# Optimization experiments

Hardware: AMD Instinct MI355X
Metric: run time of the kernel (lower is better)

The kernel has to match this reference:

```python
import jax, jax.numpy as jnp
import numpy as np

N_NODES = 100000
N_EDGES = 3200000
D_IN = 128
D_OUT = 128


def setup_inputs() -> dict:
    key = jax.random.key(0)
    k1, k2, k3, k4, k5 = jax.random.split(key, 5)
    input_feature = jax.random.normal(k1, (N_NODES, D_IN), dtype=jnp.float32)
    edge_src = jax.random.randint(k2, (N_EDGES,), 0, N_NODES, dtype=jnp.int32)
    edge_dst = jax.random.randint(k3, (N_EDGES,), 0, N_NODES, dtype=jnp.int32)
    edge_vals = jax.random.uniform(k4, (N_EDGES,), dtype=jnp.float32)
    # kaiming-uniform-like init for weight, zeros for bias (as in reset_parameters)
    bound = float(np.sqrt(6.0 / D_IN))
    weight = jax.random.uniform(k5, (D_IN, D_OUT), dtype=jnp.float32,
                                minval=-bound, maxval=bound)
    bias = jnp.zeros((D_OUT,), dtype=jnp.float32)
    return {
        "input_feature": input_feature,
        "edge_src": edge_src,
        "edge_dst": edge_dst,
        "edge_vals": edge_vals,
        "weight": weight,
        "bias": bias,
    }


def reference(input_feature, edge_src, edge_dst, edge_vals, weight, bias):
    # support = X @ W  -> [N, D_OUT]
    support = jnp.matmul(input_feature, weight)
    # sparse.mm(A, support): out[dst] += A[dst, src] * support[src]
    gathered = support[edge_src] * edge_vals[:, None]  # [E, D_OUT]
    output = jax.ops.segment_sum(gathered, edge_dst, num_segments=N_NODES)
    output = output + bias  # bias-add (use_bias=True)
    return output
```

## Files before the change

### kernel.cpp

```cpp
#include <hip/hip_runtime.h>

#define N_NODES 100000
#define N_EDGES 3200000
#define D 128

#define K1C    391
#define CHUNK  4096
#define NCHUNK 782
#define GEMMB  782
#define CAPB   8960

static const size_t OFF_SB    = 0;
static const size_t OFF_REC   = 25600000;
static const size_t OFF_SORT2 = 53626880;
static const size_t OFF_OFFS  = 67640320;
static const size_t OFF_GCUR  = 68040320;

typedef __attribute__((ext_vector_type(8))) short bf16x8;
typedef __attribute__((ext_vector_type(4))) float f32x4;

__device__ __forceinline__ unsigned short f2bf(float f) {
    unsigned u = __float_as_uint(f);
    return (unsigned short)((u + 0x7FFFu + ((u >> 16) & 1u)) >> 16);
}

__global__ __launch_bounds__(512) void part_and_gemm(
        const int* __restrict__ esrc,
        const int* __restrict__ edst,
        const float* __restrict__ eval,
        int* __restrict__ gcursor,
        int2* __restrict__ rec_out,
        const float* __restrict__ X,
        const float* __restrict__ W,
        unsigned* __restrict__ Sb) {
    __shared__ __align__(16) union {
        unsigned short wfrag[8][4][64][8];
        unsigned       stage[8][16][68];
        struct {
            int2 staged[CHUNK];
            unsigned short bkt[CHUNK];
            int hist[K1C];
            int lofs[K1C];
            int gbase[K1C];
            int cur[K1C];
            int wsum[8];
        } p;
    } u;

    const int t    = threadIdx.x;
    const int lane = t & 63;
    const int wave = t >> 6;

    if (blockIdx.x < NCHUNK) {
        const int e0  = blockIdx.x * CHUNK;
        const int cnt = min(CHUNK, N_EDGES - e0);
        const int nq  = cnt >> 2;

        for (int i = t; i < K1C; i += 512) u.p.hist[i] = 0;
        __syncthreads();

        for (int i = t; i < nq; i += 512) {
            int4 d4 = ((const int4*)(edst + e0))[i];
            atomicAdd(&u.p.hist[d4.x >> 8], 1);
            atomicAdd(&u.p.hist[d4.y >> 8], 1);
            atomicAdd(&u.p.hist[d4.z >> 8], 1);
            atomicAdd(&u.p.hist[d4.w >> 8], 1);
        }
        __syncthreads();

        int hv   = (t < K1C) ? u.p.hist[t] : 0;
        int incl = hv;
        for (int off = 1; off < 64; off <<= 1) {
            int uu = __shfl_up(incl, off);
            if (lane >= off) incl += uu;
        }
        if (lane == 63) u.p.wsum[wave] = incl;
        __syncthreads();
        {
            int pre = 0;
            for (int w = 0; w < wave; ++w) pre += u.p.wsum[w];
            if (t < K1C) {
                int excl = pre + incl - hv;
                u.p.lofs[t]  = excl;
                u.p.cur[t]   = excl;
                u.p.gbase[t] = hv ? (t * CAPB + atomicAdd(&gcursor[t], hv)) : 0;
            }
        }
        __syncthreads();

        for (int i = t; i < nq; i += 512) {
            int4   d4 = ((const int4*)(edst + e0))[i];
            int4   s4 = ((const int4*)(esrc + e0))[i];
            float4 v4 = ((const float4*)(eval + e0))[i];
            {
                int b = d4.x >> 8;
                int pos = atomicAdd(&u.p.cur[b], 1);
                u.p.staged[pos] = make_int2(s4.x | ((d4.x & 255) << 17),
                                            __float_as_int(v4.x));
                u.p.bkt[pos] = (unsigned short)b;
            }
            {
                int b = d4.y >> 8;
                int pos = atomicAdd(&u.p.cur[b], 1);
                u.p.staged[pos] = make_int2(s4.y | ((d4.y & 255) << 17),
                                            __float_as_int(v4.y));
                u.p.bkt[pos] = (unsigned short)b;
            }
            {
                int b = d4.z >> 8;
                int pos = atomicAdd(&u.p.cur[b], 1);
                u.p.staged[pos] = make_int2(s4.z | ((d4.z & 255) << 17),
                                            __float_as_int(v4.z));
                u.p.bkt[pos] = (unsigned short)b;
            }
            {
                int b = d4.w >> 8;
                int pos = atomicAdd(&u.p.cur[b], 1);
                u.p.staged[pos] = make_int2(s4.w | ((d4.w & 255) << 17),
                                            __float_as_int(v4.w));
                u.p.bkt[pos] = (unsigned short)b;
            }
        }
        __syncthreads();

        for (int i = t; i < cnt; i += 512) {
            int bb = u.p.bkt[i];
            rec_out[u.p.gbase[bb] + (i - u.p.lofs[bb])] = u.p.staged[i];
        }
    } else {
        const int quad = lane >> 4;
        const int li   = lane & 15;
        const int rowBase = (blockIdx.x - NCHUNK) * 128;

        for (int i = t; i < D * D; i += 512) {
            int k = i >> 7, n = i & 127;
            u.wfrag[n >> 4][k >> 5][((k >> 3) & 3) * 16 + (n & 15)][k & 7] = f2bf(W[i]);
        }
        __syncthreads();

        f32x4 acc[8];
#pragma unroll
        for (int ct = 0; ct < 8; ++ct)
            acc[ct] = (f32x4){0.f, 0.f, 0.f, 0.f};

#pragma unroll
        for (int kt = 0; kt < 4; ++kt) {
            int row = rowBase + wave * 16 + li;
            if (row >= N_NODES) row = N_NODES - 1;
            const float* xp = X + (size_t)row * D + kt * 32 + quad * 8;
            float4 f0 = ((const float4*)xp)[0];
            float4 f1 = ((const float4*)xp)[1];
            bf16x8 a;
            a[0] = (short)f2bf(f0.x); a[1] = (short)f2bf(f0.y);
            a[2] = (short)f2bf(f0.z); a[3] = (short)f2bf(f0.w);
            a[4] = (short)f2bf(f1.x); a[5] = (short)f2bf(f1.y);
            a[6] = (short)f2bf(f1.z); a[7] = (short)f2bf(f1.w);
#pragma unroll
            for (int ct = 0; ct < 8; ++ct) {
                bf16x8 b = *(const bf16x8*)&u.wfrag[ct][kt][lane][0];
                acc[ct] = __builtin_amdgcn_mfma_f32_16x16x32_bf16(a, b, acc[ct], 0, 0, 0);
            }
        }
        __syncthreads();

        unsigned short* sw = (unsigned short*)&u.stage[wave][0][0];
#pragma unroll
        for (int r = 0; r < 4; ++r) {
            int lrow = quad * 4 + r;
#pragma unroll
            for (int ct = 0; ct < 8; ++ct)
                sw[lrow * 136 + ct * 16 + li] = f2bf(acc[ct][r]);
        }
        for (int lrow = 0; lrow < 16; ++lrow) {
            int node = rowBase + wave * 16 + lrow;
            if (node < N_NODES)
                Sb[(size_t)node * 64 + lane] = ((unsigned*)sw)[lrow * 68 + lane];
        }
    }
}

__global__ __launch_bounds__(512) void fine_sort(
        const int2* __restrict__ rec,
        const int* __restrict__ gcnt,
        int* __restrict__ offs,
        unsigned* __restrict__ sorted1) {
    __shared__ int fh[256];
    __shared__ int fcur[256];
    __shared__ int fwsum[4];

    const int c    = blockIdx.x;
    const int t    = threadIdx.x;
    const int lane = t & 63;
    const int beg  = c * CAPB;
    const int bcnt = gcnt[c];
    const int np   = bcnt >> 1;

    if (t < 256) fh[t] = 0;
    __syncthreads();

    for (int i = t; i < np; i += 512) {
        int4 q = ((const int4*)(rec + beg))[i];
        atomicAdd(&fh[(q.x >> 17) & 255], 1);
        atomicAdd(&fh[(q.z >> 17) & 255], 1);
    }
    if (t == 0 && (bcnt & 1))
        atomicAdd(&fh[(rec[beg + bcnt - 1].x >> 17) & 255], 1);
    __syncthreads();

    if (t < 256) {
        int hv   = fh[t];
        int incl = hv;
        for (int off = 1; off < 64; off <<= 1) {
            int uu = __shfl_up(incl, off);
            if (lane >= off) incl += uu;
        }
        if (lane == 63) fwsum[t >> 6] = incl;
        fh[t] = incl - hv;
    }
    __syncthreads();
    if (t < 256) {
        int pre = 0;
        for (int w = 0; w < (t >> 6); ++w) pre += fwsum[w];
        int excl = pre + fh[t];
        int node = c * 256 + t;
        if (node < N_NODES) offs[node] = beg + excl;
        fcur[t] = beg + excl;
    }
    __syncthreads();

    for (int i = t; i < np; i += 512) {
        int4 q = ((const int4*)(rec + beg))[i];
        {
            int dl = (q.x >> 17) & 255;
            int p = atomicAdd(&fcur[dl], 1);
            unsigned vb = f2bf(__int_as_float(q.y));
            sorted1[p] = (unsigned)(q.x & 0x1FFFF) | ((vb & 0x7FFFu) << 17);
        }
        {
            int dl = (q.z >> 17) & 255;
            int p = atomicAdd(&fcur[dl], 1);
            unsigned vb = f2bf(__int_as_float(q.w));
            sorted1[p] = (unsigned)(q.z & 0x1FFFF) | ((vb & 0x7FFFu) << 17);
        }
    }
    if (t == 0 && (bcnt & 1)) {
        int2 q = rec[beg + bcnt - 1];
        int dl = (q.x >> 17) & 255;
        int p = atomicAdd(&fcur[dl], 1);
        unsigned vb = f2bf(__int_as_float(q.y));
        sorted1[p] = (unsigned)(q.x & 0x1FFFF) | ((vb & 0x7FFFu) << 17);
    }
}

#define FMA8(v, p) {                                                         \
    a0 += (v) * __uint_as_float((p).x << 16);                                \
    a1 += (v) * __uint_as_float((p).x & 0xFFFF0000u);                        \
    a2 += (v) * __uint_as_float((p).y << 16);                                \
    a3 += (v) * __uint_as_float((p).y & 0xFFFF0000u);                        \
    a4 += (v) * __uint_as_float((p).z << 16);                                \
    a5 += (v) * __uint_as_float((p).z & 0xFFFF0000u);                        \
    a6 += (v) * __uint_as_float((p).w << 16);                                \
    a7 += (v) * __uint_as_float((p).w & 0xFFFF0000u);                        \
}

__global__ __launch_bounds__(256) void reduce_segments(
        const unsigned* __restrict__ Sb,
        const unsigned* __restrict__ sorted,
        const int* __restrict__ offs,
        const int* __restrict__ gcnt,
        const float* __restrict__ bias,
        float* __restrict__ out) {
    const int lane = threadIdx.x & 63;
    const int node = (blockIdx.x * 256 + threadIdx.x) >> 6;
    if (node >= N_NODES) return;

    const int qr = lane >> 4;
    const int ql = lane & 15;

    const int beg = offs[node];
    const bool blast = ((node & 255) == 255) || (node == N_NODES - 1);
    const int end = blast ? ((node >> 8) * CAPB + gcnt[node >> 8])
                          : offs[node + 1];

    float a0 = 0.f, a1 = 0.f, a2 = 0.f, a3 = 0.f;
    float a4 = 0.f, a5 = 0.f, a6 = 0.f, a7 = 0.f;

    for (int base = beg; base < end; base += 64) {
        const int m = min(64, end - base);
        unsigned rec = 0;
        if (base + lane < end) rec = sorted[base + lane];
        const int ng = (m + 3) >> 2;

        int g = 0;
        for (; g + 4 <= ng; g += 4) {
            int i0 = 4 * (g + 0) + qr, i1 = 4 * (g + 1) + qr;
            int i2 = 4 * (g + 2) + qr, i3 = 4 * (g + 3) + qr;
            unsigned r0 = (unsigned)__shfl((int)rec, i0);
            unsigned r1 = (unsigned)__shfl((int)rec, i1);
            unsigned r2 = (unsigned)__shfl((int)rec, i2);
            unsigned r3 = (unsigned)__shfl((int)rec, i3);
            int s0 = r0 & 0x1FFFF, s1 = r1 & 0x1FFFF;
            int s2 = r2 & 0x1FFFF, s3 = r3 & 0x1FFFF;
            float v0 = __uint_as_float((r0 >> 17) << 16);
            float v1 = __uint_as_float((r1 >> 17) << 16);
            float v2 = __uint_as_float((r2 >> 17) << 16);
            float v3 = __uint_as_float((r3 >> 17) << 16);
            uint4 p0 = ((const uint4*)(Sb + (size_t)s0 * 64))[ql];
            uint4 p1 = ((const uint4*)(Sb + (size_t)s1 * 64))[ql];
            uint4 p2 = ((const uint4*)(Sb + (size_t)s2 * 64))[ql];
            uint4 p3 = ((const uint4*)(Sb + (size_t)s3 * 64))[ql];
            FMA8(v0, p0);
            FMA8(v1, p1);
            FMA8(v2, p2);
            FMA8(v3, p3);
        }
        for (; g < ng; ++g) {
            int i0 = 4 * g + qr;
            unsigned r0 = (unsigned)__shfl((int)rec, i0);
            int s0 = r0 & 0x1FFFF;
            float v0 = __uint_as_float((r0 >> 17) << 16);
            uint4 p0 = ((const uint4*)(Sb + (size_t)s0 * 64))[ql];
            FMA8(v0, p0);
        }
    }

    a0 += __shfl(a0, lane ^ 16); a1 += __shfl(a1, lane ^ 16);
    a2 += __shfl(a2, lane ^ 16); a3 += __shfl(a3, lane ^ 16);
    a4 += __shfl(a4, lane ^ 16); a5 += __shfl(a5, lane ^ 16);
    a6 += __shfl(a6, lane ^ 16); a7 += __shfl(a7, lane ^ 16);
    a0 += __shfl(a0, lane ^ 32); a1 += __shfl(a1, lane ^ 32);
    a2 += __shfl(a2, lane ^ 32); a3 += __shfl(a3, lane ^ 32);
    a4 += __shfl(a4, lane ^ 32); a5 += __shfl(a5, lane ^ 32);
    a6 += __shfl(a6, lane ^ 32); a7 += __shfl(a7, lane ^ 32);

    if (qr == 0) {
        float4 b0 = ((const float4*)bias)[2 * ql];
        float4 b1 = ((const float4*)bias)[2 * ql + 1];
        float4 r0 = make_float4(a0 + b0.x, a1 + b0.y, a2 + b0.z, a3 + b0.w);
        float4 r1 = make_float4(a4 + b1.x, a5 + b1.y, a6 + b1.z, a7 + b1.w);
        ((float4*)(out + (size_t)node * D))[2 * ql]     = r0;
        ((float4*)(out + (size_t)node * D))[2 * ql + 1] = r1;
    }
}

extern "C" void kernel_launch(void* const* d_in, const int* in_sizes, int n_in,
                              void* d_out, int out_size, void* d_ws, size_t ws_size,
                              hipStream_t stream) {
    const float* X    = (const float*)d_in[0];
    const int*   esrc = (const int*)  d_in[1];
    const int*   edst = (const int*)  d_in[2];
    const float* eval = (const float*)d_in[3];
    const float* W    = (const float*)d_in[4];
    const float* bias = (const float*)d_in[5];
    float* out = (float*)d_out;

    char* ws = (char*)d_ws;
    unsigned* SbU   = (unsigned*)(ws + OFF_SB);
    int2*     recs  = (int2*)    (ws + OFF_REC);
    unsigned* srt1  = (unsigned*)(ws + OFF_SORT2);
    int*      offs  = (int*)     (ws + OFF_OFFS);
    int*      gcur  = (int*)     (ws + OFF_GCUR);

    hipMemsetAsync(gcur, 0, K1C * 4, stream);

    part_and_gemm<<<NCHUNK + GEMMB, 512, 0, stream>>>(
        esrc, edst, eval, gcur, recs, X, W, SbU);

    fine_sort<<<K1C, 512, 0, stream>>>(recs, gcur, offs, srt1);

    reduce_segments<<<(N_NODES + 3) / 4, 256, 0, stream>>>(
        SbU, srt1, offs, gcur, bias, out);
}
```

Baseline: 289.1 us.

## Count per-node degrees with global atomics in partition pass, drop fine histogram

After: 390.5 us. +35.1%, slower.

```diff
diff --git a/kernel.cpp b/kernel.cpp
--- a/kernel.cpp
+++ b/kernel.cpp
@@ -14,7 +14,7 @@
 static const size_t OFF_REC   = 25600000;
 static const size_t OFF_SORT2 = 53626880;
 static const size_t OFF_OFFS  = 67640320;
-static const size_t OFF_GCUR  = 68040320;
+static const size_t OFF_CNTS  = 68040320;
 
 typedef __attribute__((ext_vector_type(8))) short bf16x8;
 typedef __attribute__((ext_vector_type(4))) float f32x4;
@@ -28,6 +28,7 @@
         const int* __restrict__ esrc,
         const int* __restrict__ edst,
         const float* __restrict__ eval,
+        int* __restrict__ nodecnt,
         int* __restrict__ gcursor,
         int2* __restrict__ rec_out,
         const float* __restrict__ X,
@@ -56,15 +57,43 @@
         const int cnt = min(CHUNK, N_EDGES - e0);
         const int nq  = cnt >> 2;
 
+        const bool hasA = (t < nq);
+        const bool hasB = (t + 512 < nq);
+        int4 d4a, s4a; float4 v4a;
+        int4 d4b, s4b; float4 v4b;
+        if (hasA) {
+            d4a = ((const int4*)(edst + e0))[t];
+            s4a = ((const int4*)(esrc + e0))[t];
+            v4a = ((const float4*)(eval + e0))[t];
+        }
+        if (hasB) {
+            d4b = ((const int4*)(edst + e0))[t + 512];
+            s4b = ((const int4*)(esrc + e0))[t + 512];
+            v4b = ((const float4*)(eval + e0))[t + 512];
+        }
+
         for (int i = t; i < K1C; i += 512) u.p.hist[i] = 0;
         __syncthreads();
 
-        for (int i = t; i < nq; i += 512) {
-            int4 d4 = ((const int4*)(edst + e0))[i];
-            atomicAdd(&u.p.hist[d4.x >> 8], 1);
-            atomicAdd(&u.p.hist[d4.y >> 8], 1);
-            atomicAdd(&u.p.hist[d4.z >> 8], 1);
-            atomicAdd(&u.p.hist[d4.w >> 8], 1);
+        if (hasA) {
+            atomicAdd(&u.p.hist[d4a.x >> 8], 1);
+            atomicAdd(&u.p.hist[d4a.y >> 8], 1);
+            atomicAdd(&u.p.hist[d4a.z >> 8], 1);
+            atomicAdd(&u.p.hist[d4a.w >> 8], 1);
+            atomicAdd(&nodecnt[d4a.x], 1);
+            atomicAdd(&nodecnt[d4a.y], 1);
+            atomicAdd(&nodecnt[d4a.z], 1);
+            atomicAdd(&nodecnt[d4a.w], 1);
+        }
+        if (hasB) {
+            atomicAdd(&u.p.hist[d4b.x >> 8], 1);
+            atomicAdd(&u.p.hist[d4b.y >> 8], 1);
+            atomicAdd(&u.p.hist[d4b.z >> 8], 1);
+            atomicAdd(&u.p.hist[d4b.w >> 8], 1);
+            atomicAdd(&nodecnt[d4b.x], 1);
+            atomicAdd(&nodecnt[d4b.y], 1);
+            atomicAdd(&nodecnt[d4b.z], 1);
+            atomicAdd(&nodecnt[d4b.w], 1);
         }
         __syncthreads();
 
@@ -88,36 +117,63 @@
         }
         __syncthreads();
 
-        for (int i = t; i < nq; i += 512) {
-            int4   d4 = ((const int4*)(edst + e0))[i];
-            int4   s4 = ((const int4*)(esrc + e0))[i];
-            float4 v4 = ((const float4*)(eval + e0))[i];
-            {
-                int b = d4.x >> 8;
-                int pos = atomicAdd(&u.p.cur[b], 1);
-                u.p.staged[pos] = make_int2(s4.x | ((d4.x & 255) << 17),
-                                            __float_as_int(v4.x));
-                u.p.bkt[pos] = (unsigned short)b;
-            }
-            {
-                int b = d4.y >> 8;
-                int pos = atomicAdd(&u.p.cur[b], 1);
-                u.p.staged[pos] = make_int2(s4.y | ((d4.y & 255) << 17),
-                                            __float_as_int(v4.y));
-                u.p.bkt[pos] = (unsigned short)b;
-            }
-            {
-                int b = d4.z >> 8;
-                int pos = atomicAdd(&u.p.cur[b], 1);
-                u.p.staged[pos] = make_int2(s4.z | ((d4.z & 255) << 17),
-                                            __float_as_int(v4.z));
-                u.p.bkt[pos] = (unsigned short)b;
-            }
-            {
-                int b = d4.w >> 8;
-                int pos = atomicAdd(&u.p.cur[b], 1);
-                u.p.staged[pos] = make_int2(s4.w | ((d4.w & 255) << 17),
-                                            __float_as_int(v4.w));
+        if (hasA) {
+            {
+                int b = d4a.x >> 8;
+                int pos = atomicAdd(&u.p.cur[b], 1);
+                u.p.staged[pos] = make_int2(s4a.x | ((d4a.x & 255) << 17),
+                                            __float_as_int(v4a.x));
+                u.p.bkt[pos] = (unsigned short)b;
+            }
+            {
+                int b = d4a.y >> 8;
+                int pos = atomicAdd(&u.p.cur[b], 1);
+                u.p.staged[pos] = make_int2(s4a.y | ((d4a.y & 255) << 17),
+                                            __float_as_int(v4a.y));
+                u.p.bkt[pos] = (unsigned short)b;
+            }
+            {
+                int b = d4a.z >> 8;
+                int pos = atomicAdd(&u.p.cur[b], 1);
+                u.p.staged[pos] = make_int2(s4a.z | ((d4a.z & 255) << 17),
+                                            __float_as_int(v4a.z));
+                u.p.bkt[pos] = (unsigned short)b;
+            }
+            {
+                int b = d4a.w >> 8;
+                int pos = atomicAdd(&u.p.cur[b], 1);
+                u.p.staged[pos] = make_int2(s4a.w | ((d4a.w & 255) << 17),
+                                            __float_as_int(v4a.w));
+                u.p.bkt[pos] = (unsigned short)b;
+            }
+        }
+        if (hasB) {
+            {
+                int b = d4b.x >> 8;
+                int pos = atomicAdd(&u.p.cur[b], 1);
+                u.p.staged[pos] = make_int2(s4b.x | ((d4b.x & 255) << 17),
+                                            __float_as_int(v4b.x));
+                u.p.bkt[pos] = (unsigned short)b;
+            }
+            {
+                int b = d4b.y >> 8;
+                int pos = atomicAdd(&u.p.cur[b], 1);
+                u.p.staged[pos] = make_int2(s4b.y | ((d4b.y & 255) << 17),
+                                            __float_as_int(v4b.y));
+                u.p.bkt[pos] = (unsigned short)b;
+            }
+            {
+                int b = d4b.z >> 8;
+                int pos = atomicAdd(&u.p.cur[b], 1);
+                u.p.staged[pos] = make_int2(s4b.z | ((d4b.z & 255) << 17),
+                                            __float_as_int(v4b.z));
+                u.p.bkt[pos] = (unsigned short)b;
+            }
+            {
+                int b = d4b.w >> 8;
+                int pos = atomicAdd(&u.p.cur[b], 1);
+                u.p.staged[pos] = make_int2(s4b.w | ((d4b.w & 255) << 17),
+                                            __float_as_int(v4b.w));
                 u.p.bkt[pos] = (unsigned short)b;
             }
         }
@@ -182,10 +238,11 @@
 __global__ __launch_bounds__(512) void fine_sort(
         const int2* __restrict__ rec,
         const int* __restrict__ gcnt,
+        const int* __restrict__ nodecnt,
         int* __restrict__ offs,
         unsigned* __restrict__ sorted1) {
-    __shared__ int fh[256];
     __shared__ int fcur[256];
+    __shared__ int fex[256];
     __shared__ int fwsum[4];
 
     const int c    = blockIdx.x;
@@ -195,33 +252,22 @@
     const int bcnt = gcnt[c];
     const int np   = bcnt >> 1;
 
-    if (t < 256) fh[t] = 0;
-    __syncthreads();
-
-    for (int i = t; i < np; i += 512) {
-        int4 q = ((const int4*)(rec + beg))[i];
-        atomicAdd(&fh[(q.x >> 17) & 255], 1);
-        atomicAdd(&fh[(q.z >> 17) & 255], 1);
-    }
-    if (t == 0 && (bcnt & 1))
-        atomicAdd(&fh[(rec[beg + bcnt - 1].x >> 17) & 255], 1);
-    __syncthreads();
-
     if (t < 256) {
-        int hv   = fh[t];
+        int node = c * 256 + t;
+        int hv   = (node < N_NODES) ? nodecnt[node] : 0;
         int incl = hv;
         for (int off = 1; off < 64; off <<= 1) {
             int uu = __shfl_up(incl, off);
             if (lane >= off) incl += uu;
         }
         if (lane == 63) fwsum[t >> 6] = incl;
-        fh[t] = incl - hv;
+        fex[t] = incl - hv;
     }
     __syncthreads();
     if (t < 256) {
         int pre = 0;
         for (int w = 0; w < (t >> 6); ++w) pre += fwsum[w];
-        int excl = pre + fh[t];
+        int excl = pre + fex[t];
         int node = c * 256 + t;
         if (node < N_NODES) offs[node] = beg + excl;
         fcur[t] = beg + excl;
@@ -359,14 +405,15 @@
     int2*     recs  = (int2*)    (ws + OFF_REC);
     unsigned* srt1  = (unsigned*)(ws + OFF_SORT2);
     int*      offs  = (int*)     (ws + OFF_OFFS);
-    int*      gcur  = (int*)     (ws + OFF_GCUR);
-
-    hipMemsetAsync(gcur, 0, K1C * 4, stream);
+    int*      ncnt  = (int*)     (ws + OFF_CNTS);
+    int*      gcur  = ncnt + N_NODES;
+
+    hipMemsetAsync(ncnt, 0, (N_NODES + K1C) * 4, stream);
 
     part_and_gemm<<<NCHUNK + GEMMB, 512, 0, stream>>>(
-        esrc, edst, eval, gcur, recs, X, W, SbU);
-
-    fine_sort<<<K1C, 512, 0, stream>>>(recs, gcur, offs, srt1);
+        esrc, edst, eval, ncnt, gcur, recs, X, W, SbU);
+
+    fine_sort<<<K1C, 512, 0, stream>>>(recs, gcur, ncnt, offs, srt1);
 
     reduce_segments<<<(N_NODES + 3) / 4, 256, 0, stream>>>(
         SbU, srt1, offs, gcur, bias, out);
```
